# Optimization experiments

Hardware: AMD Instinct MI355X
Metric: run time of the kernel (lower is better)

Reference implementation:

```python
import jax, jax.numpy as jnp
import numpy as np

B, D_IN, H, C = 8192, 3072, 2000, 10


def binarized(x):
    # deterministic Binarize: sign(x) scaled by mean |x| (matches quant_mode='det', allow_scale=True)
    return jnp.sign(x) * jnp.mean(jnp.abs(x))


def setup_inputs() -> dict:
    key = jax.random.key(0)
    ks = jax.random.split(key, 6)

    def lin(k, out_f, in_f):
        # torch nn.Linear default init: U(-1/sqrt(in_f), 1/sqrt(in_f))
        bound = 1.0 / np.sqrt(in_f)
        kw, kb = jax.random.split(k)
        W = jax.random.uniform(kw, (out_f, in_f), minval=-bound, maxval=bound, dtype=jnp.float32)
        b = jax.random.uniform(kb, (out_f,), minval=-bound, maxval=bound, dtype=jnp.float32)
        return W, b

    x = jax.random.normal(ks[0], (B, D_IN), dtype=jnp.float32)
    W1, b1 = lin(ks[1], H, D_IN)
    W2, b2 = lin(ks[2], H, H)
    W3, b3 = lin(ks[3], H, H)
    W4, b4 = lin(ks[4], H, H)
    W5, b5 = lin(ks[5], C, H)
    return {"x": x, "W1": W1, "b1": b1, "W2": W2, "b2": b2,
            "W3": W3, "b3": b3, "W4": W4, "b4": b4, "W5": W5, "b5": b5}


def reference(x, W1, b1, W2, b2, W3, b3, W4, b4, W5, b5):
    # layer 1: binary_a==1 but layer_index==1 -> input NOT binarized; weight binarized
    h = jax.nn.relu(x @ binarized(W1).T + b1)
    # layers 2-4: binarize both activations and weights
    h = jax.nn.relu(binarized(h) @ binarized(W2).T + b2)
    h = jax.nn.relu(binarized(h) @ binarized(W3).T + b3)
    h = jax.nn.relu(binarized(h) @ binarized(W4).T + b4)
    # fc1 is a plain fp32 Linear
    return h @ W5.T + b5
```

## Files before the change

kernel.cpp:

```cpp
#include <hip/hip_runtime.h>
#include <hip/hip_bf16.h>
#include <stdint.h>

typedef __bf16 bf16_t;
typedef __attribute__((ext_vector_type(8))) __bf16 bf16x8;
typedef __attribute__((ext_vector_type(4))) float f32x4;
typedef __attribute__((ext_vector_type(4))) int i32x4;
typedef __attribute__((ext_vector_type(8))) char i8x8;

#define GLD_LDS16(g, l) __builtin_amdgcn_global_load_lds( \
    (__attribute__((address_space(1))) void*)(g), \
    (__attribute__((address_space(3))) void*)(l), 16, 0, 0)

__device__ __forceinline__ void block_reduce_atomic_d(double v, double* dst) {
    #pragma unroll
    for (int off = 32; off > 0; off >>= 1) v += __shfl_down(v, off);
    __shared__ double rb[4];
    const int t = threadIdx.x;
    if ((t & 63) == 0) rb[t >> 6] = v;
    __syncthreads();
    if (t == 0) atomicAdd(dst, rb[0] + rb[1] + rb[2] + rb[3]);
}

__global__ __launch_bounds__(256) void prep_w(
    const float* __restrict__ W, int rows, int cols,
    bf16_t* __restrict__ S, int ldS, int halfW, int dupOff,
    double* __restrict__ sumOut)
{
    const int r = blockIdx.x;
    const int t = threadIdx.x;
    double sl = 0.0;
    for (int cb = t * 8; cb < halfW; cb += 2048) {
        bf16x8 o;
        if (r < rows) {
            #pragma unroll
            for (int j = 0; j < 8; ++j) {
                int c = cb + j;
                float v = (c < cols) ? W[(size_t)r * cols + c] : 0.f;
                sl += (double)fabsf(v);
                o[j] = (bf16_t)(v > 0.f ? 1.f : (v < 0.f ? -1.f : 0.f));
            }
        } else {
            #pragma unroll
            for (int j = 0; j < 8; ++j) o[j] = (bf16_t)0.f;
        }
        *(bf16x8*)&S[(size_t)r * ldS + cb] = o;
        if (dupOff) *(bf16x8*)&S[(size_t)r * ldS + dupOff + cb] = o;
    }
    block_reduce_atomic_d(sl, sumOut);
}

__global__ __launch_bounds__(256) void prep_w_i8(
    const float* __restrict__ W, int rows, int cols,
    int8_t* __restrict__ S, double* __restrict__ sumOut)
{
    const int r = blockIdx.x;
    const int t = threadIdx.x;
    const int cb = t * 8;
    double sl = 0.0;
    i8x8 o;
    if (r < rows) {
        #pragma unroll
        for (int j = 0; j < 8; ++j) {
            int c = cb + j;
            float v = (c < cols) ? W[(size_t)r * cols + c] : 0.f;
            sl += (double)fabsf(v);
            o[j] = (char)(v > 0.f ? 1 : (v < 0.f ? -1 : 0));
        }
    } else {
        #pragma unroll
        for (int j = 0; j < 8; ++j) o[j] = 0;
    }
    *(i8x8*)&S[(size_t)r * 2048 + cb] = o;
    block_reduce_atomic_d(sl, sumOut);
}

__global__ __launch_bounds__(256) void prep_x(
    const float* __restrict__ x, bf16_t* __restrict__ XLi, bf16_t* __restrict__ XLr)
{
    const int r = blockIdx.x, t = threadIdx.x;
    for (int cb = t * 8; cb < 3072; cb += 2048) {
        float4 v0 = *(const float4*)&x[(size_t)r * 3072 + cb];
        float4 v1 = *(const float4*)&x[(size_t)r * 3072 + cb + 4];
        float xv[8] = {v0.x, v0.y, v0.z, v0.w, v1.x, v1.y, v1.z, v1.w};
        bf16x8 hi, lo, re;
        #pragma unroll
        for (int j = 0; j < 8; ++j) {
            int Q = (int)lrintf(xv[j] * 16384.f);
            int d0 = ((Q + 256) & 511) - 256;
            int d1 = (Q - d0) / 512;
            float rr = xv[j] - (float)Q * (1.f / 16384.f);
            hi[j] = (bf16_t)(float)(d1 * 512);
            lo[j] = (bf16_t)(float)d0;
            re[j] = (bf16_t)(rr * 16384.f);
        }
        *(bf16x8*)&XLi[(size_t)r * 6144 + cb]        = hi;
        *(bf16x8*)&XLi[(size_t)r * 6144 + 3072 + cb] = lo;
        *(bf16x8*)&XLr[(size_t)r * 3072 + cb]        = re;
    }
}

__global__ __launch_bounds__(256, 4) void gemm_bin(
    const bf16_t* __restrict__ A, const bf16_t* __restrict__ B, int K, int ldB,
    float* __restrict__ rawOut,
    const float* __restrict__ addPlane,
    const double* __restrict__ sumW, double invDivW, double extraScale,
    const float* __restrict__ bias,
    int8_t* __restrict__ binOut,
    double* __restrict__ habs)
{
    __shared__ __align__(16) bf16_t sA[128 * 64];
    __shared__ __align__(16) bf16_t sB[128 * 64];
    const int t = threadIdx.x;
    const int lane = t & 63;
    const int wave = t >> 6;
    const int wr = wave >> 1, wc = wave & 1;
    const int qa = lane >> 4, rA = lane & 15;
    const size_t bm = (size_t)blockIdx.y * 128, bn = (size_t)blockIdx.x * 128;

    f32x4 acc[4][4] = {};

    const bf16_t* Abase = A + bm * (size_t)K;
    const bf16_t* Bbase = B + bn * (size_t)ldB;

    const int swz = rA & 7;
    const int offk0 = ((0 + qa) ^ swz) * 8;
    const int offk1 = ((4 + qa) ^ swz) * 8;
    const int arow = wr * 64 + rA;
    const int brow = wc * 64 + rA;

    for (int k0 = 0; k0 < K; k0 += 64) {
        #pragma unroll
        for (int i = 0; i < 4; ++i) {
            int c = i * 256 + t;
            int row = c >> 3, cc = c & 7;
            int ccg = cc ^ (row & 7);
            GLD_LDS16(Abase + (size_t)row * K + k0 + ccg * 8, &sA[c * 8]);
        }
        #pragma unroll
        for (int i = 0; i < 4; ++i) {
            int c = i * 256 + t;
            int row = c >> 3, cc = c & 7;
            int ccg = cc ^ (row & 7);
            GLD_LDS16(Bbase + (size_t)row * ldB + k0 + ccg * 8, &sB[c * 8]);
        }
        __syncthreads();

        bf16x8 fa[4][2], fb[4][2];
        #pragma unroll
        for (int i = 0; i < 4; ++i) {
            fa[i][0] = *(const bf16x8*)&sA[(arow + i * 16) * 64 + offk0];
            fa[i][1] = *(const bf16x8*)&sA[(arow + i * 16) * 64 + offk1];
            fb[i][0] = *(const bf16x8*)&sB[(brow + i * 16) * 64 + offk0];
            fb[i][1] = *(const bf16x8*)&sB[(brow + i * 16) * 64 + offk1];
        }
        #pragma unroll
        for (int i = 0; i < 4; ++i)
            #pragma unroll
            for (int j = 0; j < 4; ++j) {
                acc[i][j] = __builtin_amdgcn_mfma_f32_16x16x32_bf16(fa[i][0], fb[j][0], acc[i][j], 0, 0, 0);
                acc[i][j] = __builtin_amdgcn_mfma_f32_16x16x32_bf16(fa[i][1], fb[j][1], acc[i][j], 0, 0, 0);
            }
        __syncthreads();
    }

    if (rawOut) {
        #pragma unroll
        for (int i = 0; i < 4; ++i)
            #pragma unroll
            for (int j = 0; j < 4; ++j)
                #pragma unroll
                for (int rr = 0; rr < 4; ++rr) {
                    int m = (int)bm + wr * 64 + i * 16 + qa * 4 + rr;
                    int n = (int)bn + wc * 64 + j * 16 + rA;
                    rawOut[(size_t)m * 2048 + n] = acc[i][j][rr];
                }
        return;
    }

    const double scale = sumW[0] * invDivW * extraScale;
    double hs = 0.0;
    #pragma unroll
    for (int i = 0; i < 4; ++i) {
        #pragma unroll
        for (int j = 0; j < 4; ++j) {
            #pragma unroll
            for (int rr = 0; rr < 4; ++rr) {
                int m = (int)bm + wr * 64 + i * 16 + qa * 4 + rr;
                int n = (int)bn + wc * 64 + j * 16 + rA;
                size_t idx = (size_t)m * 2048 + n;
                double s = (double)acc[i][j][rr];
                if (addPlane) s += (double)addPlane[idx];
                double z = s * scale + (n < 2000 ? (double)bias[n] : -1.0);
                binOut[idx] = (int8_t)(z > 0.0 ? 1 : 0);
                if (n < 2000 && z > 0.0) hs += z;
            }
        }
    }
    if (habs) block_reduce_atomic_d(hs, habs);
}

__global__ __launch_bounds__(256, 4) void gemm_i8(
    const int8_t* __restrict__ A, const int8_t* __restrict__ B,
    const double* __restrict__ sumW, double invDivW,
    const double* __restrict__ sumH, double invDivH,
    const float* __restrict__ bias,
    int8_t* __restrict__ binOut, bf16_t* __restrict__ hOut,
    double* __restrict__ habs)
{
    const int K = 2048;
    __shared__ __align__(16) int8_t sA[128 * 128];
    __shared__ __align__(16) int8_t sB[128 * 128];
    const int t = threadIdx.x;
    const int lane = t & 63;
    const int wave = t >> 6;
    const int wr = wave >> 1, wc = wave & 1;
    const int qa = lane >> 4, rA = lane & 15;
    const size_t bm = (size_t)blockIdx.y * 128, bn = (size_t)blockIdx.x * 128;

    i32x4 acc[4][4] = {};

    const int8_t* Abase = A + bm * (size_t)K;
    const int8_t* Bbase = B + bn * (size_t)K;

    const int swz = rA & 7;
    const int offb0 = ((0 + qa) ^ swz) * 16;
    const int offb1 = ((4 + qa) ^ swz) * 16;
    const int arow = wr * 64 + rA;
    const int brow = wc * 64 + rA;

    for (int k0 = 0; k0 < K; k0 += 128) {
        #pragma unroll
        for (int i = 0; i < 4; ++i) {
            int c = i * 256 + t;
            int row = c >> 3, cc = c & 7;
            int ccg = cc ^ (row & 7);
            GLD_LDS16(Abase + (size_t)row * K + k0 + ccg * 16, &sA[c * 16]);
        }
        #pragma unroll
        for (int i = 0; i < 4; ++i) {
            int c = i * 256 + t;
            int row = c >> 3, cc = c & 7;
            int ccg = cc ^ (row & 7);
            GLD_LDS16(Bbase + (size_t)row * K + k0 + ccg * 16, &sB[c * 16]);
        }
        __syncthreads();

        i32x4 fa[4][2], fb[4][2];
        #pragma unroll
        for (int i = 0; i < 4; ++i) {
            fa[i][0] = *(const i32x4*)&sA[(arow + i * 16) * 128 + offb0];
            fa[i][1] = *(const i32x4*)&sA[(arow + i * 16) * 128 + offb1];
            fb[i][0] = *(const i32x4*)&sB[(brow + i * 16) * 128 + offb0];
            fb[i][1] = *(const i32x4*)&sB[(brow + i * 16) * 128 + offb1];
        }
        #pragma unroll
        for (int i = 0; i < 4; ++i)
            #pragma unroll
            for (int j = 0; j < 4; ++j) {
                acc[i][j] = __builtin_amdgcn_mfma_i32_16x16x64_i8(fa[i][0], fb[j][0], acc[i][j], 0, 0, 0);
                acc[i][j] = __builtin_amdgcn_mfma_i32_16x16x64_i8(fa[i][1], fb[j][1], acc[i][j], 0, 0, 0);
            }
        __syncthreads();
    }

    const double scale = sumW[0] * invDivW * sumH[0] * invDivH;
    double hs = 0.0;
    #pragma unroll
    for (int i = 0; i < 4; ++i) {
        #pragma unroll
        for (int j = 0; j < 4; ++j) {
            #pragma unroll
            for (int rr = 0; rr < 4; ++rr) {
                int m = (int)bm + wr * 64 + i * 16 + qa * 4 + rr;
                int n = (int)bn + wc * 64 + j * 16 + rA;
                size_t idx = (size_t)m * 2048 + n;
                double z = (double)acc[i][j][rr] * scale +
                           (n < 2000 ? (double)bias[n] : -1.0);
                if (binOut) binOut[idx] = (int8_t)(z > 0.0 ? 1 : 0);
                if (hOut)   hOut[idx] = (bf16_t)(float)(z > 0.0 ? z : 0.0);
                if (n < 2000 && z > 0.0) hs += z;
            }
        }
    }
    if (habs) block_reduce_atomic_d(hs, habs);
}

__global__ __launch_bounds__(256) void fc_final(
    const bf16_t* __restrict__ h4, const float* __restrict__ W5,
    const float* __restrict__ b5, float* __restrict__ out)
{
    const int r = blockIdx.x, t = threadIdx.x;
    float acc[10] = {};
    for (int k = t; k < 2000; k += 256) {
        float a = (float)h4[(size_t)r * 2048 + k];
        #pragma unroll
        for (int c = 0; c < 10; ++c) acc[c] += a * W5[c * 2000 + k];
    }
    __shared__ float red[4][10];
    #pragma unroll
    for (int c = 0; c < 10; ++c) {
        float v = acc[c];
        #pragma unroll
        for (int off = 32; off > 0; off >>= 1) v += __shfl_down(v, off);
        if ((t & 63) == 0) red[t >> 6][c] = v;
    }
    __syncthreads();
    if (t < 10) out[(size_t)r * 10 + t] = red[0][t] + red[1][t] + red[2][t] + red[3][t] + b5[t];
}

extern "C" void kernel_launch(void* const* d_in, const int* in_sizes, int n_in,
                              void* d_out, int out_size, void* d_ws, size_t ws_size,
                              hipStream_t stream)
{
    const float* x  = (const float*)d_in[0];
    const float* W1 = (const float*)d_in[1];
    const float* b1 = (const float*)d_in[2];
    const float* W2 = (const float*)d_in[3];
    const float* b2 = (const float*)d_in[4];
    const float* W3 = (const float*)d_in[5];
    const float* b3 = (const float*)d_in[6];
    const float* W4 = (const float*)d_in[7];
    const float* b4 = (const float*)d_in[8];
    const float* W5 = (const float*)d_in[9];
    const float* b5 = (const float*)d_in[10];
    float* out = (float*)d_out;
    (void)ws_size; (void)in_sizes; (void)n_in; (void)out_size;

    const size_t PH = (size_t)8192 * 2048;

    char* w = (char*)d_ws;
    double* scD = (double*)w;
    size_t off = 256;
    bf16_t* XLi = (bf16_t*)(w + off); off += (size_t)8192 * 6144 * 2;
    bf16_t* XLr = (bf16_t*)(w + off); off += (size_t)8192 * 3072 * 2;
    bf16_t* sW1 = (bf16_t*)(w + off); off += (size_t)2048 * 6144 * 2;
    float*  Ti  = (float*)(w + off);  off += PH * 4;
    int8_t* p0  = (int8_t*)(w + off); off += PH;
    int8_t* sW2 = (int8_t*)XLi;
    int8_t* sW3 = sW2 + (size_t)2048 * 2048;
    int8_t* sW4 = sW3 + (size_t)2048 * 2048;
    int8_t* p1  = sW4 + (size_t)2048 * 2048;
    bf16_t* h4  = (bf16_t*)Ti;

    hipMemsetAsync(w, 0, 256, stream);
    prep_w<<<2048, 256, 0, stream>>>(W1, 2000, 3072, sW1, 6144, 3072, 3072, scD + 0);
    prep_x<<<8192, 256, 0, stream>>>(x, XLi, XLr);

    dim3 grid(16, 64), blk(256);
    gemm_bin<<<grid, blk, 0, stream>>>(XLi, sW1, 6144, 6144, Ti, nullptr,
                                       nullptr, 0.0, 1.0, nullptr, nullptr, nullptr);
    gemm_bin<<<grid, blk, 0, stream>>>(XLr, sW1, 3072, 6144, nullptr, Ti,
                                       scD + 0, 1.0 / 6144000.0, 1.0 / 16384.0,
                                       b1, p0, scD + 4);
    prep_w_i8<<<2048, 256, 0, stream>>>(W2, 2000, 2000, sW2, scD + 1);
    prep_w_i8<<<2048, 256, 0, stream>>>(W3, 2000, 2000, sW3, scD + 2);
    prep_w_i8<<<2048, 256, 0, stream>>>(W4, 2000, 2000, sW4, scD + 3);

    gemm_i8<<<grid, blk, 0, stream>>>(p0, sW2,
                                      scD + 1, 1.0 / 4000000.0, scD + 4, 1.0 / 16384000.0,
                                      b2, p1, nullptr, scD + 5);
    gemm_i8<<<grid, blk, 0, stream>>>(p1, sW3,
                                      scD + 2, 1.0 / 4000000.0, scD + 5, 1.0 / 16384000.0,
                                      b3, p0, nullptr, scD + 6);
    gemm_i8<<<grid, blk, 0, stream>>>(p0, sW4,
                                      scD + 3, 1.0 / 4000000.0, scD + 6, 1.0 / 16384000.0,
                                      b4, nullptr, h4, nullptr);
    fc_final<<<8192, 256, 0, stream>>>(h4, W5, b5, out);
}
```

Before: 910.3 us.

## Fuse all weight and input prep into one kernel and split int8 MFMA fragment loads

Merges the W1 bf16 prep, the three int8 weight preps and the x split into a single prep_all launch. sW2-4 move to their own workspace region and p1 now aliases XLi, so the int8 weight preps no longer have to wait for the layer-1 GEMMs. The int8 GEMM inner loop is split into two half-K passes with separate fragment arrays to reduce register pressure. The fused launch removes four launches and their serialization, at the cost of a larger workspace footprint.

```diff
diff --git a/kernel.cpp b/kernel.cpp
--- a/kernel.cpp
+++ b/kernel.cpp
@@ -22,21 +22,17 @@
     if (t == 0) atomicAdd(dst, rb[0] + rb[1] + rb[2] + rb[3]);
 }
 
-__global__ __launch_bounds__(256) void prep_w(
-    const float* __restrict__ W, int rows, int cols,
-    bf16_t* __restrict__ S, int ldS, int halfW, int dupOff,
-    double* __restrict__ sumOut)
-{
-    const int r = blockIdx.x;
+__device__ __forceinline__ void prep_w1_row(
+    const float* __restrict__ W, int r, bf16_t* __restrict__ S, double* sumOut)
+{
     const int t = threadIdx.x;
     double sl = 0.0;
-    for (int cb = t * 8; cb < halfW; cb += 2048) {
+    for (int cb = t * 8; cb < 3072; cb += 2048) {
         bf16x8 o;
-        if (r < rows) {
+        if (r < 2000) {
             #pragma unroll
             for (int j = 0; j < 8; ++j) {
-                int c = cb + j;
-                float v = (c < cols) ? W[(size_t)r * cols + c] : 0.f;
+                float v = W[(size_t)r * 3072 + cb + j];
                 sl += (double)fabsf(v);
                 o[j] = (bf16_t)(v > 0.f ? 1.f : (v < 0.f ? -1.f : 0.f));
             }
@@ -44,26 +40,24 @@
             #pragma unroll
             for (int j = 0; j < 8; ++j) o[j] = (bf16_t)0.f;
         }
-        *(bf16x8*)&S[(size_t)r * ldS + cb] = o;
-        if (dupOff) *(bf16x8*)&S[(size_t)r * ldS + dupOff + cb] = o;
+        *(bf16x8*)&S[(size_t)r * 6144 + cb] = o;
+        *(bf16x8*)&S[(size_t)r * 6144 + 3072 + cb] = o;
     }
     block_reduce_atomic_d(sl, sumOut);
 }
 
-__global__ __launch_bounds__(256) void prep_w_i8(
-    const float* __restrict__ W, int rows, int cols,
-    int8_t* __restrict__ S, double* __restrict__ sumOut)
-{
-    const int r = blockIdx.x;
+__device__ __forceinline__ void prep_wi8_row(
+    const float* __restrict__ W, int r, int8_t* __restrict__ S, double* sumOut)
+{
     const int t = threadIdx.x;
     const int cb = t * 8;
     double sl = 0.0;
     i8x8 o;
-    if (r < rows) {
+    if (r < 2000) {
         #pragma unroll
         for (int j = 0; j < 8; ++j) {
             int c = cb + j;
-            float v = (c < cols) ? W[(size_t)r * cols + c] : 0.f;
+            float v = (c < 2000) ? W[(size_t)r * 2000 + c] : 0.f;
             sl += (double)fabsf(v);
             o[j] = (char)(v > 0.f ? 1 : (v < 0.f ? -1 : 0));
         }
@@ -75,10 +69,10 @@
     block_reduce_atomic_d(sl, sumOut);
 }
 
-__global__ __launch_bounds__(256) void prep_x(
-    const float* __restrict__ x, bf16_t* __restrict__ XLi, bf16_t* __restrict__ XLr)
-{
-    const int r = blockIdx.x, t = threadIdx.x;
+__device__ __forceinline__ void prep_x_row(
+    const float* __restrict__ x, int r, bf16_t* __restrict__ XLi, bf16_t* __restrict__ XLr)
+{
+    const int t = threadIdx.x;
     for (int cb = t * 8; cb < 3072; cb += 2048) {
         float4 v0 = *(const float4*)&x[(size_t)r * 3072 + cb];
         float4 v1 = *(const float4*)&x[(size_t)r * 3072 + cb + 4];
@@ -98,6 +92,23 @@
         *(bf16x8*)&XLi[(size_t)r * 6144 + 3072 + cb] = lo;
         *(bf16x8*)&XLr[(size_t)r * 3072 + cb]        = re;
     }
+}
+
+__global__ __launch_bounds__(256) void prep_all(
+    const float* __restrict__ W1, const float* __restrict__ W2,
+    const float* __restrict__ W3, const float* __restrict__ W4,
+    const float* __restrict__ x,
+    bf16_t* __restrict__ sW1, int8_t* __restrict__ sW2,
+    int8_t* __restrict__ sW3, int8_t* __restrict__ sW4,
+    bf16_t* __restrict__ XLi, bf16_t* __restrict__ XLr,
+    double* __restrict__ scD)
+{
+    const int g = blockIdx.x;
+    if      (g < 2048)  prep_w1_row(W1, g, sW1, scD + 0);
+    else if (g < 4096)  prep_wi8_row(W2, g - 2048, sW2, scD + 1);
+    else if (g < 6144)  prep_wi8_row(W3, g - 4096, sW3, scD + 2);
+    else if (g < 8192)  prep_wi8_row(W4, g - 6144, sW4, scD + 3);
+    else                prep_x_row(x, g - 8192, XLi, XLr);
 }
 
 __global__ __launch_bounds__(256, 4) void gemm_bin(
@@ -246,21 +257,32 @@
         }
         __syncthreads();
 
-        i32x4 fa[4][2], fb[4][2];
-        #pragma unroll
-        for (int i = 0; i < 4; ++i) {
-            fa[i][0] = *(const i32x4*)&sA[(arow + i * 16) * 128 + offb0];
-            fa[i][1] = *(const i32x4*)&sA[(arow + i * 16) * 128 + offb1];
-            fb[i][0] = *(const i32x4*)&sB[(brow + i * 16) * 128 + offb0];
-            fb[i][1] = *(const i32x4*)&sB[(brow + i * 16) * 128 + offb1];
-        }
-        #pragma unroll
-        for (int i = 0; i < 4; ++i)
-            #pragma unroll
-            for (int j = 0; j < 4; ++j) {
-                acc[i][j] = __builtin_amdgcn_mfma_i32_16x16x64_i8(fa[i][0], fb[j][0], acc[i][j], 0, 0, 0);
-                acc[i][j] = __builtin_amdgcn_mfma_i32_16x16x64_i8(fa[i][1], fb[j][1], acc[i][j], 0, 0, 0);
-            }
+        {
+            i32x4 fa[4], fb[4];
+            #pragma unroll
+            for (int i = 0; i < 4; ++i) {
+                fa[i] = *(const i32x4*)&sA[(arow + i * 16) * 128 + offb0];
+                fb[i] = *(const i32x4*)&sB[(brow + i * 16) * 128 + offb0];
+            }
+            #pragma unroll
+            for (int i = 0; i < 4; ++i)
+                #pragma unroll
+                for (int j = 0; j < 4; ++j)
+                    acc[i][j] = __builtin_amdgcn_mfma_i32_16x16x64_i8(fa[i], fb[j], acc[i][j], 0, 0, 0);
+        }
+        {
+            i32x4 fa[4], fb[4];
+            #pragma unroll
+            for (int i = 0; i < 4; ++i) {
+                fa[i] = *(const i32x4*)&sA[(arow + i * 16) * 128 + offb1];
+                fb[i] = *(const i32x4*)&sB[(brow + i * 16) * 128 + offb1];
+            }
+            #pragma unroll
+            for (int i = 0; i < 4; ++i)
+                #pragma unroll
+                for (int j = 0; j < 4; ++j)
+                    acc[i][j] = __builtin_amdgcn_mfma_i32_16x16x64_i8(fa[i], fb[j], acc[i][j], 0, 0, 0);
+        }
         __syncthreads();
     }
 
@@ -337,15 +359,15 @@
     bf16_t* sW1 = (bf16_t*)(w + off); off += (size_t)2048 * 6144 * 2;
     float*  Ti  = (float*)(w + off);  off += PH * 4;
     int8_t* p0  = (int8_t*)(w + off); off += PH;
-    int8_t* sW2 = (int8_t*)XLi;
-    int8_t* sW3 = sW2 + (size_t)2048 * 2048;
-    int8_t* sW4 = sW3 + (size_t)2048 * 2048;
-    int8_t* p1  = sW4 + (size_t)2048 * 2048;
+    int8_t* sW2 = (int8_t*)(w + off); off += (size_t)2048 * 2048;
+    int8_t* sW3 = (int8_t*)(w + off); off += (size_t)2048 * 2048;
+    int8_t* sW4 = (int8_t*)(w + off); off += (size_t)2048 * 2048;
+    int8_t* p1  = (int8_t*)XLi;
     bf16_t* h4  = (bf16_t*)Ti;
 
     hipMemsetAsync(w, 0, 256, stream);
-    prep_w<<<2048, 256, 0, stream>>>(W1, 2000, 3072, sW1, 6144, 3072, 3072, scD + 0);
-    prep_x<<<8192, 256, 0, stream>>>(x, XLi, XLr);
+    prep_all<<<16384, 256, 0, stream>>>(W1, W2, W3, W4, x,
+                                        sW1, sW2, sW3, sW4, XLi, XLr, scD);
 
     dim3 grid(16, 64), blk(256);
     gemm_bin<<<grid, blk, 0, stream>>>(XLi, sW1, 6144, 6144, Ti, nullptr,
@@ -353,9 +375,6 @@
     gemm_bin<<<grid, blk, 0, stream>>>(XLr, sW1, 3072, 6144, nullptr, Ti,
                                        scD + 0, 1.0 / 6144000.0, 1.0 / 16384.0,
                                        b1, p0, scD + 4);
-    prep_w_i8<<<2048, 256, 0, stream>>>(W2, 2000, 2000, sW2, scD + 1);
-    prep_w_i8<<<2048, 256, 0, stream>>>(W3, 2000, 2000, sW3, scD + 2);
-    prep_w_i8<<<2048, 256, 0, stream>>>(W4, 2000, 2000, sW4, scD + 3);
 
     gemm_i8<<<grid, blk, 0, stream>>>(p0, sW2,
                                       scD + 1, 1.0 / 4000000.0, scD + 4, 1.0 / 16384000.0,
```

Result: faster. 853.9 us (-6.2%).
